# Performance work log

Hardware: AMD Instinct MI355X
Metric: run time of the kernel (lower is better)

## Reference

```python
import jax, jax.numpy as jnp
import numpy as np

N, B, D = 2048, 2, 512
H, R = 8, 3
C = D // H  # head dim = 64


def setup_inputs() -> dict:
    key = jax.random.key(0)
    ks = jax.random.split(key, 12)
    x_q = jax.random.normal(ks[0], (N, B, D), jnp.float32)
    x_k = jax.random.normal(ks[1], (N, B, D), jnp.float32)
    x_v = jax.random.normal(ks[2], (N, B, D), jnp.float32)
    attn_mask = jax.random.randint(ks[3], (B, R, N, N), 0, 2).astype(bool)
    # pad the last 128 key positions (realistic padding; avoids all -inf rows)
    key_padding_mask = jnp.zeros((B, N), bool).at[:, -128:].set(True)
    s = 1.0 / np.sqrt(D)
    Wq = jax.random.normal(ks[4], (D, D), jnp.float32) * s
    Wk = jax.random.normal(ks[5], (D, D), jnp.float32) * s
    Wv = jax.random.normal(ks[6], (D, D), jnp.float32) * s
    Wo = jax.random.normal(ks[7], (D, D), jnp.float32) * s
    bq = jnp.zeros((D,), jnp.float32)
    bk = jnp.zeros((D,), jnp.float32)
    bv = jnp.zeros((D,), jnp.float32)
    bo = jnp.zeros((D,), jnp.float32)
    # mask_weight: randn, last column set to sqrt(head_dim) as in __init__
    mask_weight = jax.random.normal(ks[8], (H, R + 1), jnp.float32)
    mask_weight = mask_weight.at[:, -1].set(np.sqrt(C))
    return dict(x_q=x_q, x_k=x_k, x_v=x_v, attn_mask=attn_mask,
                key_padding_mask=key_padding_mask, Wq=Wq, bq=bq, Wk=Wk, bk=bk,
                Wv=Wv, bv=bv, Wo=Wo, bo=bo, mask_weight=mask_weight)


def _split_heads(x):
    # (n, b, h*c) -> (b, h, n, c)
    n, b, _ = x.shape
    return jnp.transpose(x.reshape(n, b, H, C), (1, 2, 0, 3))


def reference(x_q, x_k, x_v, attn_mask, key_padding_mask,
              Wq, bq, Wk, bk, Wv, bv, Wo, bo, mask_weight):
    q = _split_heads(x_q @ Wq + bq)  # (b,h,n,c)
    k = _split_heads(x_k @ Wk + bk)
    v = _split_heads(x_v @ Wv + bv)

    # relative bias: softmax over edge-type weights, scaled per head
    rel_w = jax.nn.softmax(mask_weight[:, :-1], axis=-1)  # (h,r)
    inv_mask = (~attn_mask).astype(jnp.float32)           # (b,r,n,m)
    rel = jnp.einsum('hr,h,brnm->bhnm', rel_w, mask_weight[:, -1], inv_mask)
    rel = jnp.where(key_padding_mask[:, None, None, :], -jnp.inf, rel)

    # scaled dot-product attention (torch default scale = 1/sqrt(head_dim))
    scores = jnp.einsum('bhnc,bhmc->bhnm', q, k) * (1.0 / np.sqrt(C))
    attn = jax.nn.softmax(scores + rel, axis=-1)
    o = jnp.einsum('bhnm,bhmc->bhnc', attn, v)

    # (b,h,n,c) -> (n,b,h*c)
    n = o.shape[2]
    o = jnp.transpose(o, (2, 0, 1, 3)).reshape(n, o.shape[0], H * C)
    return o @ Wo + bo
```

## Files before the change

kernel.cpp:

```cpp
#include <hip/hip_runtime.h>
#include <hip/hip_bf16.h>

#define NN 2048
#define LOG2E 1.4426950408889634f

typedef unsigned int u32;
typedef unsigned short u16;
typedef unsigned char u8;

typedef __attribute__((ext_vector_type(8))) short short8;
typedef __attribute__((ext_vector_type(4))) float f32x4;

__device__ __forceinline__ u16 f2bf(float f){
  __hip_bfloat16 h = __float2bfloat16(f);
  return *reinterpret_cast<u16*>(&h);
}
__device__ __forceinline__ u32 pack2(float a, float b){
  return (u32)f2bf(a) | ((u32)f2bf(b) << 16);
}

__global__ __launch_bounds__(256)
void prep_k(const int* __restrict__ am, const int* __restrict__ kp,
            u8* __restrict__ cmb)
{
  const size_t tid  = (size_t)blockIdx.x * 256 + threadIdx.x;
  const size_t base = tid * 4;
  const int row = (int)(base >> 11);
  const int m0  = (int)(base & 2047);
  const int b = row >> 11, n = row & 2047;
  const size_t e0 = (((size_t)(b*3) * NN) + n) * NN + m0;
  const int4 a0 = *reinterpret_cast<const int4*>(am + e0);
  const int4 a1 = *reinterpret_cast<const int4*>(am + e0 + (size_t)NN*NN);
  const int4 a2 = *reinterpret_cast<const int4*>(am + e0 + 2*(size_t)NN*NN);
  const int4 kv = *reinterpret_cast<const int4*>(kp + (size_t)b*NN + m0);
  const int a0v[4] = {a0.x,a0.y,a0.z,a0.w};
  const int a1v[4] = {a1.x,a1.y,a1.z,a1.w};
  const int a2v[4] = {a2.x,a2.y,a2.z,a2.w};
  const int kvv[4] = {kv.x,kv.y,kv.z,kv.w};
  uchar4 out;
  u8* o = (u8*)&out;
  #pragma unroll
  for (int i = 0; i < 4; ++i)
    o[i] = (u8)((a0v[i]?1:0) | (a1v[i]?2:0) | (a2v[i]?4:0) | (kvv[i]?8:0));
  *reinterpret_cast<uchar4*>(cmb + base) = out;
}

__global__ __launch_bounds__(256)
void trw_k(const float* __restrict__ W, u16* __restrict__ WT)
{
  __shared__ float tile[32][33];
  const int t = threadIdx.x;
  const int k0 = blockIdx.x * 32, n0 = blockIdx.y * 32;
  const int c = t & 31, r = t >> 5;
  #pragma unroll
  for (int i = 0; i < 4; ++i)
    tile[r + 8*i][c] = W[(size_t)(k0 + r + 8*i) * 512 + n0 + c];
  __syncthreads();
  #pragma unroll
  for (int i = 0; i < 4; ++i)
    WT[(size_t)(n0 + r + 8*i) * 512 + k0 + c] = f2bf(tile[c][r + 8*i]);
}

template<int BN, bool SCATTER, bool ABF16, bool OUTF32>
__device__ __forceinline__
void gemm_core(const void* __restrict__ Av, const u16* __restrict__ WT,
               const float* __restrict__ bias, void* __restrict__ Cd,
               float scale, int m0, int n0)
{
  constexpr int NI  = BN / 64;
  constexpr int WNL = BN / 32;
  __shared__ u16 As[2][64*64];
  __shared__ u16 Ws[2][BN*64];

  const int t = threadIdx.x;
  const int lane = t & 63;
  const int w = t >> 6;
  const int g = lane >> 4, r15 = lane & 15;
  const int wn = w * (BN/4);

  const int arow = t >> 2, akc = (t & 3) * 16, as0 = (t & 3) * 2;
  const int wrn = (BN==128) ? (t>>1) : (t>>2);
  const int wkc = (BN==128) ? ((t&1)*32) : ((t&3)*16);
  const int wsb = (BN==128) ? ((t&1)*4)  : ((t&3)*2);

  uint4  war[WNL];
  uint4  aab[2];
  float4 aaf[4];

  auto loadA = [&](int k0){
    if constexpr (ABF16) {
      const u16* A = (const u16*)Av;
      aab[0] = *reinterpret_cast<const uint4*>(A + (size_t)(m0+arow)*512 + k0 + akc);
      aab[1] = *reinterpret_cast<const uint4*>(A + (size_t)(m0+arow)*512 + k0 + akc + 8);
    } else {
      const float* A = (const float*)Av;
      #pragma unroll
      for (int q = 0; q < 4; ++q)
        aaf[q] = *reinterpret_cast<const float4*>(A + (size_t)(m0+arow)*512 + k0 + akc + 4*q);
    }
  };
  auto loadW = [&](int k0){
    #pragma unroll
    for (int i = 0; i < WNL; ++i)
      war[i] = *reinterpret_cast<const uint4*>(WT + (size_t)(n0+wrn)*512 + k0 + wkc + 8*i);
  };
  auto writeA = [&](int bf){
    uint4 v0, v1;
    if constexpr (ABF16) { v0 = aab[0]; v1 = aab[1]; }
    else {
      v0.x = pack2(aaf[0].x, aaf[0].y); v0.y = pack2(aaf[0].z, aaf[0].w);
      v0.z = pack2(aaf[1].x, aaf[1].y); v0.w = pack2(aaf[1].z, aaf[1].w);
      v1.x = pack2(aaf[2].x, aaf[2].y); v1.y = pack2(aaf[2].z, aaf[2].w);
      v1.z = pack2(aaf[3].x, aaf[3].y); v1.w = pack2(aaf[3].z, aaf[3].w);
    }
    *reinterpret_cast<uint4*>(&As[bf][arow*64 + (((as0  ) ^ (arow&7)) << 3)]) = v0;
    *reinterpret_cast<uint4*>(&As[bf][arow*64 + (((as0+1) ^ (arow&7)) << 3)]) = v1;
  };
  auto writeW = [&](int bf){
    #pragma unroll
    for (int i = 0; i < WNL; ++i)
      *reinterpret_cast<uint4*>(&Ws[bf][wrn*64 + (((wsb+i) ^ (wrn&7)) << 3)]) = war[i];
  };

  const f32x4 fz = {0.f,0.f,0.f,0.f};
  f32x4 acc[4][NI];
  #pragma unroll
  for (int mi = 0; mi < 4; ++mi)
    #pragma unroll
    for (int ni = 0; ni < NI; ++ni) acc[mi][ni] = fz;

  loadA(0); loadW(0);
  writeA(0); writeW(0);
  __syncthreads();

  for (int kt = 0; kt < 8; ++kt) {
    const int cur = kt & 1;
    if (kt < 7) { loadA((kt+1)*64); loadW((kt+1)*64); }
    #pragma unroll
    for (int ks = 0; ks < 2; ++ks) {
      short8 bfr[NI], afr[4];
      #pragma unroll
      for (int ni = 0; ni < NI; ++ni) {
        const int n = wn + 16*ni + r15;
        bfr[ni] = *reinterpret_cast<const short8*>(&Ws[cur][n*64 + (((ks*4+g) ^ (n&7)) << 3)]);
      }
      #pragma unroll
      for (int mi = 0; mi < 4; ++mi) {
        const int m = 16*mi + r15;
        afr[mi] = *reinterpret_cast<const short8*>(&As[cur][m*64 + (((ks*4+g) ^ (m&7)) << 3)]);
      }
      #pragma unroll
      for (int mi = 0; mi < 4; ++mi)
        #pragma unroll
        for (int ni = 0; ni < NI; ++ni)
          acc[mi][ni] = __builtin_amdgcn_mfma_f32_16x16x32_bf16(afr[mi], bfr[ni], acc[mi][ni], 0, 0, 0);
    }
    if (kt < 7) { writeA(cur^1); writeW(cur^1); }
    __syncthreads();
  }

  float bia[NI];
  #pragma unroll
  for (int ni = 0; ni < NI; ++ni) bia[ni] = bias[n0 + wn + 16*ni + r15];
  #pragma unroll
  for (int mi = 0; mi < 4; ++mi) {
    #pragma unroll
    for (int ni = 0; ni < NI; ++ni) {
      #pragma unroll
      for (int j = 0; j < 4; ++j) {
        const int row = m0 + 16*mi + 4*g + j;
        const int col = n0 + wn + 16*ni + r15;
        const float v = (acc[mi][ni][j] + bia[ni]) * scale;
        if constexpr (SCATTER) {
          const int bb = row & 1, ntok = row >> 1;
          const int h = col >> 6, c = col & 63;
          ((u16*)Cd)[(((size_t)(bb*8 + h) * NN + ntok) * 64) + c] = f2bf(v);
        } else if constexpr (OUTF32) {
          ((float*)Cd)[(size_t)row * 512 + col] = v;
        } else {
          ((u16*)Cd)[(size_t)row * 512 + col] = f2bf(v);
        }
      }
    }
  }
}

__global__ __launch_bounds__(256)
void gemm_qkv(const float* __restrict__ x0, const float* __restrict__ x1,
              const float* __restrict__ x2, const u16* __restrict__ WT3,
              const float* __restrict__ b0, const float* __restrict__ b1,
              const float* __restrict__ b2, u16* __restrict__ dst, float qscale)
{
  const int z = blockIdx.z;
  const float* A    = (z == 0) ? x0 : (z == 1) ? x1 : x2;
  const float* bias = (z == 0) ? b0 : (z == 1) ? b1 : b2;
  gemm_core<128, true, false, false>(A, WT3 + (size_t)z*262144, bias,
                                     dst + (size_t)z*2097152,
                                     (z == 0) ? qscale : 1.0f,
                                     blockIdx.x*64, blockIdx.y*128);
}

__global__ __launch_bounds__(256)
void gemm_wo(const u16* __restrict__ Ob, const u16* __restrict__ WT,
             const float* __restrict__ bias, float* __restrict__ out)
{
  gemm_core<64, false, true, true>(Ob, WT, bias, out, 1.0f,
                                   blockIdx.x*64, blockIdx.y*64);
}

__global__ __launch_bounds__(512)
void attn_mfma(const u16* __restrict__ Q, const u16* __restrict__ K,
               const u16* __restrict__ V, const u8* __restrict__ cmb,
               const float* __restrict__ mw, u16* __restrict__ O,
               float* __restrict__ Opart, float2* __restrict__ Ml, int kspan)
{
  __shared__ u16 Ks[2][64*64];
  __shared__ u16 Vs[2][64*64];
  __shared__ u16 Ps[8][16*64];
  __shared__ float lut[16];

  const int t = threadIdx.x;
  const int lane = t & 63;
  const int w = t >> 6;
  const int g = lane >> 4;
  const int r15 = lane & 15;
  const int bh = blockIdx.y;
  const int z = blockIdx.z;
  const int b = bh >> 3, h = bh & 7;
  const int n0 = blockIdx.x * 128;
  const int nq = n0 + w*16 + r15;
  const int k_beg = z * kspan;
  const float NEGINF = -__builtin_inff();

  if (t < 16) {
    const float mw0 = mw[h*4+0], mw1 = mw[h*4+1], mw2 = mw[h*4+2];
    const float msc = mw[h*4+3];
    const float mxw = fmaxf(mw0, fmaxf(mw1, mw2));
    const float e0 = __expf(mw0-mxw), e1 = __expf(mw1-mxw), e2 = __expf(mw2-mxw);
    const float inv = msc / (e0+e1+e2);
    float v = ((t & 1) ? 0.f : e0*inv) + ((t & 2) ? 0.f : e1*inv)
            + ((t & 4) ? 0.f : e2*inv);
    lut[t] = (t & 8) ? NEGINF : v * LOG2E;
  }

  const u16* qrow = Q + ((size_t)bh*NN + nq)*64;
  const short8 bq0 = *reinterpret_cast<const short8*>(qrow + 8*g);
  const short8 bq1 = *reinterpret_cast<const short8*>(qrow + 32 + 8*g);

  const u8* crow = cmb + ((size_t)(b*NN + nq))*NN;
  const u16* Kbase = K + (size_t)bh*NN*64;
  const u16* Vbase = V + (size_t)bh*NN*64;

  float m_run = NEGINF, l_run = 0.f;
  const f32x4 fz = {0.f, 0.f, 0.f, 0.f};
  f32x4 oacc[4] = {fz, fz, fz, fz};

  const int sm  = t >> 3;
  const int sc0 = (t & 7) * 8;
  const int ss  = t & 7;

  uint4 kreg, vreg;
  auto loadKV = [&](int m0){
    kreg = *reinterpret_cast<const uint4*>(Kbase + (size_t)(m0 + sm)*64 + sc0);
    vreg = *reinterpret_cast<const uint4*>(Vbase + (size_t)(m0 + sm)*64 + sc0);
  };
  auto writeKV = [&](int bf){
    *reinterpret_cast<uint4*>(&Ks[bf][sm*64 + ((ss ^ (sm & 7)) << 3)]) = kreg;
    u16 e[8];
    e[0]=vreg.x&0xffff; e[1]=vreg.x>>16; e[2]=vreg.y&0xffff; e[3]=vreg.y>>16;
    e[4]=vreg.z&0xffff; e[5]=vreg.z>>16; e[6]=vreg.w&0xffff; e[7]=vreg.w>>16;
    #pragma unroll
    for (int i = 0; i < 8; ++i) {
      const int c = sc0 + i;
      Vs[bf][c*64 + ((((sm>>3) ^ (c&7) ^ (c>>3)) << 3) | (sm & 7))] = e[i];
    }
  };

  const int ntiles = kspan >> 6;
  loadKV(k_beg);
  writeKV(0);
  __syncthreads();

  for (int it = 0; it < ntiles; ++it) {
    const int cur = it & 1;
    const int m0 = k_beg + it * 64;
    const bool more = (it + 1 < ntiles);
    if (more) loadKV(m0 + 64);

    f32x4 sac[4];
    #pragma unroll
    for (int kt = 0; kt < 4; ++kt) {
      const int key = 16*kt + r15;
      const short8 a0 = *reinterpret_cast<const short8*>(&Ks[cur][key*64 + (((g  ) ^ (key&7)) << 3)]);
      const short8 a1 = *reinterpret_cast<const short8*>(&Ks[cur][key*64 + (((g+4) ^ (key&7)) << 3)]);
      f32x4 s = fz;
      s = __builtin_amdgcn_mfma_f32_16x16x32_bf16(a0, bq0, s, 0, 0, 0);
      s = __builtin_amdgcn_mfma_f32_16x16x32_bf16(a1, bq1, s, 0, 0, 0);
      sac[kt] = s;
    }

    float sv[4][4];
    float pmax = NEGINF;
    #pragma unroll
    for (int kt = 0; kt < 4; ++kt) {
      const u32 cw = *reinterpret_cast<const u32*>(crow + m0 + 16*kt + 4*g);
      #pragma unroll
      for (int j = 0; j < 4; ++j) {
        const u32 ci = (cw >> (8*j)) & 0xffu;
        sv[kt][j] = sac[kt][j] + lut[ci];
        pmax = fmaxf(pmax, sv[kt][j]);
      }
    }
    float tmax = pmax;
    tmax = fmaxf(tmax, __shfl_xor(tmax, 16));
    tmax = fmaxf(tmax, __shfl_xor(tmax, 32));

    const float nm = fmaxf(m_run, tmax);
    float sc;
    if (nm == NEGINF) { sc = 1.f; }
    else { sc = exp2f(m_run - nm); m_run = nm; }

    float psum = 0.f;
    #pragma unroll
    for (int kt = 0; kt < 4; ++kt) {
      float p[4];
      #pragma unroll
      for (int j = 0; j < 4; ++j) {
        p[j] = (nm == NEGINF) ? 0.f : exp2f(sv[kt][j] - nm);
        psum += p[j];
      }
      const int slot = 2*kt + (g >> 1);
      const int off  = 4 * (g & 1);
      *reinterpret_cast<ushort4*>(&Ps[w][r15*64 + ((slot ^ (r15 & 7)) << 3) + off]) =
        make_ushort4(f2bf(p[0]), f2bf(p[1]), f2bf(p[2]), f2bf(p[3]));
    }
    psum += __shfl_xor(psum, 16);
    psum += __shfl_xor(psum, 32);
    l_run = l_run * sc + psum;
    #pragma unroll
    for (int ct = 0; ct < 4; ++ct) oacc[ct] *= sc;

    const short8 bp0 = *reinterpret_cast<const short8*>(&Ps[w][r15*64 + (((g  ) ^ (r15 & 7)) << 3)]);
    const short8 bp1 = *reinterpret_cast<const short8*>(&Ps[w][r15*64 + (((g+4) ^ (r15 & 7)) << 3)]);
    #pragma unroll
    for (int ct = 0; ct < 4; ++ct) {
      const int c = 16*ct + r15;
      const int sw0 = (g  ) ^ (c&7) ^ (c>>3);
      const int sw1 = (g+4) ^ (c&7) ^ (c>>3);
      const short8 av0 = *reinterpret_cast<const short8*>(&Vs[cur][c*64 + (sw0 << 3)]);
      const short8 av1 = *reinterpret_cast<const short8*>(&Vs[cur][c*64 + (sw1 << 3)]);
      oacc[ct] = __builtin_amdgcn_mfma_f32_16x16x32_bf16(av0, bp0, oacc[ct], 0, 0, 0);
      oacc[ct] = __builtin_amdgcn_mfma_f32_16x16x32_bf16(av1, bp1, oacc[ct], 0, 0, 0);
    }

    if (more) writeKV(cur ^ 1);
    __syncthreads();
  }

  if (Opart) {
    float* orow = Opart + (((size_t)(z*16 + bh)) * NN + nq) * 64;
    #pragma unroll
    for (int ct = 0; ct < 4; ++ct)
      *reinterpret_cast<float4*>(orow + 16*ct + 4*g) =
        make_float4(oacc[ct][0], oacc[ct][1], oacc[ct][2], oacc[ct][3]);
    if (g == 0)
      Ml[((size_t)(z*16 + bh)) * NN + nq] = make_float2(m_run, l_run);
  } else {
    const float rinv = 1.f / l_run;
    #pragma unroll
    for (int ct = 0; ct < 4; ++ct) {
      u16* dst = O + ((size_t)(nq*2 + b))*512 + h*64 + 16*ct + 4*g;
      *reinterpret_cast<ushort4*>(dst) =
        make_ushort4(f2bf(oacc[ct][0]*rinv), f2bf(oacc[ct][1]*rinv),
                     f2bf(oacc[ct][2]*rinv), f2bf(oacc[ct][3]*rinv));
    }
  }
}

__global__ __launch_bounds__(256)
void combine_k(const float* __restrict__ Opart, const float2* __restrict__ Ml,
               u16* __restrict__ Ob, int nsplit)
{
  const int t = threadIdx.x;
  const int lane = t & 63, w = t >> 6;
  const int q = blockIdx.x * 4 + w;
  const int bh = blockIdx.y;
  const int b = bh >> 3, h = bh & 7;

  float M = -__builtin_inff();
  for (int s = 0; s < nsplit; ++s)
    M = fmaxf(M, Ml[((size_t)(s*16 + bh)) * NN + q].x);

  float num = 0.f, den = 0.f;
  for (int s = 0; s < nsplit; ++s) {
    const float2 ml = Ml[((size_t)(s*16 + bh)) * NN + q];
    const float ws = (ml.x == -__builtin_inff()) ? 0.f : exp2f(ml.x - M);
    den += ws * ml.y;
    num += ws * Opart[(((size_t)(s*16 + bh)) * NN + q) * 64 + lane];
  }
  const float r = (den > 0.f) ? num / den : 0.f;
  Ob[((size_t)(q*2 + b)) * 512 + h*64 + lane] = f2bf(r);
}

extern "C" void kernel_launch(void* const* d_in, const int* in_sizes, int n_in,
                              void* d_out, int out_size, void* d_ws, size_t ws_size,
                              hipStream_t stream)
{
  const float* xq = (const float*)d_in[0];
  const float* xk = (const float*)d_in[1];
  const float* xv = (const float*)d_in[2];
  const int*   am = (const int*)d_in[3];
  const int*   kp = (const int*)d_in[4];
  const float* Wq = (const float*)d_in[5];
  const float* bq = (const float*)d_in[6];
  const float* Wk = (const float*)d_in[7];
  const float* bk = (const float*)d_in[8];
  const float* Wv = (const float*)d_in[9];
  const float* bv = (const float*)d_in[10];
  const float* Wo = (const float*)d_in[11];
  const float* bo = (const float*)d_in[12];
  const float* mw = (const float*)d_in[13];

  u16* Qb = (u16*)d_ws;
  u16* Kb = Qb + (size_t)16*NN*64;
  u16* Vb = Kb + (size_t)16*NN*64;
  u16* Ob = Vb + (size_t)16*NN*64;
  u8*  cmb = (u8*)(Ob + (size_t)4096*512);
  u8*  R   = cmb + (size_t)2*NN*NN;

  u16*   WT3   = (u16*)R;
  float* Opart = (float*)R;
  const size_t base_bytes = (size_t)(R - (u8*)d_ws);
  int nsplit = 1;
  for (int s = 4; s >= 1; s >>= 1) {
    const size_t need = base_bytes + (size_t)s * 16 * NN * (64*4 + 8);
    if (need <= ws_size) { nsplit = s; break; }
  }
  float2* Ml = (float2*)(Opart + (size_t)nsplit * 16 * NN * 64);
  const bool split = (base_bytes + (size_t)16*NN*(64*4+8) <= ws_size) &&
                     (base_bytes + (size_t)3*512*512*2 <= ws_size);
  u16* WTo = Qb;

  prep_k<<<(2*NN*NN/4 + 255)/256, 256, 0, stream>>>(am, kp, cmb);

  const float qscale = 0.125f * LOG2E;
  if (split) {
    trw_k<<<dim3(16, 16), 256, 0, stream>>>(Wq, WT3);
    trw_k<<<dim3(16, 16), 256, 0, stream>>>(Wk, WT3 + 262144);
    trw_k<<<dim3(16, 16), 256, 0, stream>>>(Wv, WT3 + 2*262144);
    gemm_qkv<<<dim3(64, 4, 3), 256, 0, stream>>>(xq, xk, xv, WT3, bq, bk, bv, Qb, qscale);
    attn_mfma<<<dim3(16, 16, nsplit), 512, 0, stream>>>(Qb, Kb, Vb, cmb, mw, Ob,
                                                        Opart, Ml, NN / nsplit);
    combine_k<<<dim3(NN/4, 16), 256, 0, stream>>>(Opart, Ml, Ob, nsplit);
    trw_k<<<dim3(16, 16), 256, 0, stream>>>(Wo, WTo);
    gemm_wo<<<dim3(64, 8), 256, 0, stream>>>(Ob, WTo, bo, (float*)d_out);
  } else {
    trw_k<<<dim3(16, 16), 256, 0, stream>>>(Wq, WT3);
    gemm_qkv<<<dim3(64, 4, 1), 256, 0, stream>>>(xq, xk, xv, WT3, bq, bk, bv, Qb, qscale);
    trw_k<<<dim3(16, 16), 256, 0, stream>>>(Wk, WT3);
    gemm_qkv<<<dim3(64, 4, 1), 256, 0, stream>>>(xk, xk, xv, WT3 - 262144, bk, bk, bv, Kb - 0, qscale);
    attn_mfma<<<dim3(16, 16, 1), 512, 0, stream>>>(Qb, Kb, Vb, cmb, mw, Ob,
                                                   nullptr, nullptr, NN);
    trw_k<<<dim3(16, 16), 256, 0, stream>>>(Wo, WTo);
    gemm_wo<<<dim3(64, 8), 256, 0, stream>>>(Ob, WTo, bo, (float*)d_out);
  }
}
```

Before: 130.5 us.

## Rework attention inner loop: direct-to-LDS K loads, register P shuffle, lazy rescale

```diff
diff --git a/kernel.cpp b/kernel.cpp
--- a/kernel.cpp
+++ b/kernel.cpp
@@ -17,6 +17,10 @@
 }
 __device__ __forceinline__ u32 pack2(float a, float b){
   return (u32)f2bf(a) | ((u32)f2bf(b) << 16);
+}
+__device__ __forceinline__ void gload16(const void* g, void* l){
+  __builtin_amdgcn_global_load_lds((const __attribute__((address_space(1))) u32*)g,
+                                   (__attribute__((address_space(3))) u32*)l, 16, 0, 0);
 }
 
 __global__ __launch_bounds__(256)
@@ -46,6 +50,25 @@
 }
 
 __global__ __launch_bounds__(256)
+void trw3_k(const float* __restrict__ W0, const float* __restrict__ W1,
+            const float* __restrict__ W2, u16* __restrict__ WT)
+{
+  __shared__ float tile[32][33];
+  const float* W = (blockIdx.z == 0) ? W0 : (blockIdx.z == 1) ? W1 : W2;
+  u16* dst = WT + (size_t)blockIdx.z * 262144;
+  const int t = threadIdx.x;
+  const int k0 = blockIdx.x * 32, n0 = blockIdx.y * 32;
+  const int c = t & 31, r = t >> 5;
+  #pragma unroll
+  for (int i = 0; i < 4; ++i)
+    tile[r + 8*i][c] = W[(size_t)(k0 + r + 8*i) * 512 + n0 + c];
+  __syncthreads();
+  #pragma unroll
+  for (int i = 0; i < 4; ++i)
+    dst[(size_t)(n0 + r + 8*i) * 512 + k0 + c] = f2bf(tile[c][r + 8*i]);
+}
+
+__global__ __launch_bounds__(256)
 void trw_k(const float* __restrict__ W, u16* __restrict__ WT)
 {
   __shared__ float tile[32][33];
@@ -208,7 +231,7 @@
                                    blockIdx.x*64, blockIdx.y*64);
 }
 
-__global__ __launch_bounds__(512)
+__global__ __launch_bounds__(512, 8)
 void attn_mfma(const u16* __restrict__ Q, const u16* __restrict__ K,
                const u16* __restrict__ V, const u8* __restrict__ cmb,
                const float* __restrict__ mw, u16* __restrict__ O,
@@ -216,7 +239,6 @@
 {
   __shared__ u16 Ks[2][64*64];
   __shared__ u16 Vs[2][64*64];
-  __shared__ u16 Ps[8][16*64];
   __shared__ float lut[16];
 
   const int t = threadIdx.x;
@@ -256,16 +278,20 @@
   f32x4 oacc[4] = {fz, fz, fz, fz};
 
   const int sm  = t >> 3;
+  const int ssl = t & 7;
+  const int kcol = (ssl ^ (sm & 7)) * 8;
   const int sc0 = (t & 7) * 8;
-  const int ss  = t & 7;
-
-  uint4 kreg, vreg;
-  auto loadKV = [&](int m0){
-    kreg = *reinterpret_cast<const uint4*>(Kbase + (size_t)(m0 + sm)*64 + sc0);
+  const int aA = (((g & 1) << 5) + r15) << 2;
+  const int aB = aA + 64;
+
+  uint4 vreg;
+  auto gloadK = [&](int m0, int bf){
+    gload16(Kbase + (size_t)(m0 + sm)*64 + kcol, &Ks[bf][w*512 + (lane << 3)]);
+  };
+  auto loadV = [&](int m0){
     vreg = *reinterpret_cast<const uint4*>(Vbase + (size_t)(m0 + sm)*64 + sc0);
   };
-  auto writeKV = [&](int bf){
-    *reinterpret_cast<uint4*>(&Ks[bf][sm*64 + ((ss ^ (sm & 7)) << 3)]) = kreg;
+  auto writeV = [&](int bf){
     u16 e[8];
     e[0]=vreg.x&0xffff; e[1]=vreg.x>>16; e[2]=vreg.y&0xffff; e[3]=vreg.y>>16;
     e[4]=vreg.z&0xffff; e[5]=vreg.z>>16; e[6]=vreg.w&0xffff; e[7]=vreg.w>>16;
@@ -277,17 +303,18 @@
   };
 
   const int ntiles = kspan >> 6;
-  loadKV(k_beg);
-  writeKV(0);
+  gloadK(k_beg, 0);
+  loadV(k_beg);
+  writeV(0);
   __syncthreads();
 
   for (int it = 0; it < ntiles; ++it) {
     const int cur = it & 1;
     const int m0 = k_beg + it * 64;
     const bool more = (it + 1 < ntiles);
-    if (more) loadKV(m0 + 64);
-
-    f32x4 sac[4];
+    if (more) { gloadK(m0 + 64, cur ^ 1); loadV(m0 + 64); }
+
+    float sv[4][4];
     #pragma unroll
     for (int kt = 0; kt < 4; ++kt) {
       const int key = 16*kt + r15;
@@ -296,64 +323,102 @@
       f32x4 s = fz;
       s = __builtin_amdgcn_mfma_f32_16x16x32_bf16(a0, bq0, s, 0, 0, 0);
       s = __builtin_amdgcn_mfma_f32_16x16x32_bf16(a1, bq1, s, 0, 0, 0);
-      sac[kt] = s;
-    }
-
-    float sv[4][4];
+      const u32 cw = *reinterpret_cast<const u32*>(crow + m0 + 16*kt + 4*g);
+      #pragma unroll
+      for (int j = 0; j < 4; ++j)
+        sv[kt][j] = s[j] + lut[(cw >> (8*j)) & 0xfu];
+    }
     float pmax = NEGINF;
     #pragma unroll
-    for (int kt = 0; kt < 4; ++kt) {
-      const u32 cw = *reinterpret_cast<const u32*>(crow + m0 + 16*kt + 4*g);
-      #pragma unroll
-      for (int j = 0; j < 4; ++j) {
-        const u32 ci = (cw >> (8*j)) & 0xffu;
-        sv[kt][j] = sac[kt][j] + lut[ci];
-        pmax = fmaxf(pmax, sv[kt][j]);
-      }
-    }
+    for (int kt = 0; kt < 4; ++kt)
+      #pragma unroll
+      for (int j = 0; j < 4; ++j) pmax = fmaxf(pmax, sv[kt][j]);
     float tmax = pmax;
     tmax = fmaxf(tmax, __shfl_xor(tmax, 16));
     tmax = fmaxf(tmax, __shfl_xor(tmax, 32));
 
-    const float nm = fmaxf(m_run, tmax);
-    float sc;
-    if (nm == NEGINF) { sc = 1.f; }
-    else { sc = exp2f(m_run - nm); m_run = nm; }
+    const bool skip = __all((m_run != NEGINF) && (tmax <= m_run + 10.0f));
+    float nm = m_run, sc = 1.0f;
+    if (!skip) {
+      nm = fmaxf(m_run, tmax);
+      if (nm != NEGINF) { sc = exp2f(m_run - nm); m_run = nm; }
+      #pragma unroll
+      for (int ct = 0; ct < 4; ++ct) oacc[ct] *= sc;
+    }
 
     float psum = 0.f;
-    #pragma unroll
-    for (int kt = 0; kt < 4; ++kt) {
-      float p[4];
-      #pragma unroll
-      for (int j = 0; j < 4; ++j) {
-        p[j] = (nm == NEGINF) ? 0.f : exp2f(sv[kt][j] - nm);
-        psum += p[j];
-      }
-      const int slot = 2*kt + (g >> 1);
-      const int off  = 4 * (g & 1);
-      *reinterpret_cast<ushort4*>(&Ps[w][r15*64 + ((slot ^ (r15 & 7)) << 3) + off]) =
-        make_ushort4(f2bf(p[0]), f2bf(p[1]), f2bf(p[2]), f2bf(p[3]));
-    }
+    const bool hig = (g >= 2);
+
+    {
+      u32 wp[2][2];
+      #pragma unroll
+      for (int kt = 0; kt < 2; ++kt) {
+        float p[4];
+        #pragma unroll
+        for (int j = 0; j < 4; ++j) {
+          p[j] = (nm == NEGINF) ? 0.f : exp2f(sv[kt][j] - nm);
+          psum += p[j];
+        }
+        wp[kt][0] = pack2(p[0], p[1]);
+        wp[kt][1] = pack2(p[2], p[3]);
+      }
+      const u32 e0 = __builtin_amdgcn_ds_bpermute(aA, (int)wp[0][0]);
+      const u32 e1 = __builtin_amdgcn_ds_bpermute(aA, (int)wp[0][1]);
+      const u32 e2 = __builtin_amdgcn_ds_bpermute(aB, (int)wp[0][0]);
+      const u32 e3 = __builtin_amdgcn_ds_bpermute(aB, (int)wp[0][1]);
+      const u32 f0 = __builtin_amdgcn_ds_bpermute(aA, (int)wp[1][0]);
+      const u32 f1 = __builtin_amdgcn_ds_bpermute(aA, (int)wp[1][1]);
+      const u32 f2 = __builtin_amdgcn_ds_bpermute(aB, (int)wp[1][0]);
+      const u32 f3 = __builtin_amdgcn_ds_bpermute(aB, (int)wp[1][1]);
+      union { uint4 u; short8 s; } cv;
+      cv.u = make_uint4(hig ? f0 : e0, hig ? f1 : e1, hig ? f2 : e2, hig ? f3 : e3);
+      const short8 bp0 = cv.s;
+      #pragma unroll
+      for (int ct = 0; ct < 4; ++ct) {
+        const int c = 16*ct + r15;
+        const short8 av0 = *reinterpret_cast<const short8*>(
+          &Vs[cur][c*64 + ((((g  ) ^ (c&7) ^ (c>>3))) << 3)]);
+        oacc[ct] = __builtin_amdgcn_mfma_f32_16x16x32_bf16(av0, bp0, oacc[ct], 0, 0, 0);
+      }
+    }
+    {
+      u32 wp[2][2];
+      #pragma unroll
+      for (int kt = 0; kt < 2; ++kt) {
+        float p[4];
+        #pragma unroll
+        for (int j = 0; j < 4; ++j) {
+          p[j] = (nm == NEGINF) ? 0.f : exp2f(sv[kt+2][j] - nm);
+          psum += p[j];
+        }
+        wp[kt][0] = pack2(p[0], p[1]);
+        wp[kt][1] = pack2(p[2], p[3]);
+      }
+      const u32 e0 = __builtin_amdgcn_ds_bpermute(aA, (int)wp[0][0]);
+      const u32 e1 = __builtin_amdgcn_ds_bpermute(aA, (int)wp[0][1]);
+      const u32 e2 = __builtin_amdgcn_ds_bpermute(aB, (int)wp[0][0]);
+      const u32 e3 = __builtin_amdgcn_ds_bpermute(aB, (int)wp[0][1]);
+      const u32 f0 = __builtin_amdgcn_ds_bpermute(aA, (int)wp[1][0]);
+      const u32 f1 = __builtin_amdgcn_ds_bpermute(aA, (int)wp[1][1]);
+      const u32 f2 = __builtin_amdgcn_ds_bpermute(aB, (int)wp[1][0]);
+      const u32 f3 = __builtin_amdgcn_ds_bpermute(aB, (int)wp[1][1]);
+      union { uint4 u; short8 s; } cv;
+      cv.u = make_uint4(hig ? f0 : e0, hig ? f1 : e1, hig ? f2 : e2, hig ? f3 : e3);
+      const short8 bp1 = cv.s;
+      #pragma unroll
+      for (int ct = 0; ct < 4; ++ct) {
+        const int c = 16*ct + r15;
+        const short8 av1 = *reinterpret_cast<const short8*>(
+          &Vs[cur][c*64 + ((((g+4) ^ (c&7) ^ (c>>3))) << 3)]);
+        oacc[ct] = __builtin_amdgcn_mfma_f32_16x16x32_bf16(av1, bp1, oacc[ct], 0, 0, 0);
+      }
+    }
+
     psum += __shfl_xor(psum, 16);
     psum += __shfl_xor(psum, 32);
     l_run = l_run * sc + psum;
-    #pragma unroll
-    for (int ct = 0; ct < 4; ++ct) oacc[ct] *= sc;
-
-    const short8 bp0 = *reinterpret_cast<const short8*>(&Ps[w][r15*64 + (((g  ) ^ (r15 & 7)) << 3)]);
-    const short8 bp1 = *reinterpret_cast<const short8*>(&Ps[w][r15*64 + (((g+4) ^ (r15 & 7)) << 3)]);
-    #pragma unroll
-    for (int ct = 0; ct < 4; ++ct) {
-      const int c = 16*ct + r15;
-      const int sw0 = (g  ) ^ (c&7) ^ (c>>3);
-      const int sw1 = (g+4) ^ (c&7) ^ (c>>3);
-      const short8 av0 = *reinterpret_cast<const short8*>(&Vs[cur][c*64 + (sw0 << 3)]);
-      const short8 av1 = *reinterpret_cast<const short8*>(&Vs[cur][c*64 + (sw1 << 3)]);
-      oacc[ct] = __builtin_amdgcn_mfma_f32_16x16x32_bf16(av0, bp0, oacc[ct], 0, 0, 0);
-      oacc[ct] = __builtin_amdgcn_mfma_f32_16x16x32_bf16(av1, bp1, oacc[ct], 0, 0, 0);
-    }
-
-    if (more) writeKV(cur ^ 1);
+
+    if (more) writeV(cur ^ 1);
     __syncthreads();
   }
 
@@ -444,24 +509,17 @@
   prep_k<<<(2*NN*NN/4 + 255)/256, 256, 0, stream>>>(am, kp, cmb);
 
   const float qscale = 0.125f * LOG2E;
+  trw3_k<<<dim3(16, 16, 3), 256, 0, stream>>>(Wq, Wk, Wv, WT3);
+  gemm_qkv<<<dim3(64, 4, 3), 256, 0, stream>>>(xq, xk, xv, WT3, bq, bk, bv, Qb, qscale);
+
   if (split) {
-    trw_k<<<dim3(16, 16), 256, 0, stream>>>(Wq, WT3);
-    trw_k<<<dim3(16, 16), 256, 0, stream>>>(Wk, WT3 + 262144);
-    trw_k<<<dim3(16, 16), 256, 0, stream>>>(Wv, WT3 + 2*262144);
-    gemm_qkv<<<dim3(64, 4, 3), 256, 0, stream>>>(xq, xk, xv, WT3, bq, bk, bv, Qb, qscale);
     attn_mfma<<<dim3(16, 16, nsplit), 512, 0, stream>>>(Qb, Kb, Vb, cmb, mw, Ob,
                                                         Opart, Ml, NN / nsplit);
     combine_k<<<dim3(NN/4, 16), 256, 0, stream>>>(Opart, Ml, Ob, nsplit);
-    trw_k<<<dim3(16, 16), 256, 0, stream>>>(Wo, WTo);
-    gemm_wo<<<dim3(64, 8), 256, 0, stream>>>(Ob, WTo, bo, (float*)d_out);
   } else {
-    trw_k<<<dim3(16, 16), 256, 0, stream>>>(Wq, WT3);
-    gemm_qkv<<<dim3(64, 4, 1), 256, 0, stream>>>(xq, xk, xv, WT3, bq, bk, bv, Qb, qscale);
-    trw_k<<<dim3(16, 16), 256, 0, stream>>>(Wk, WT3);
-    gemm_qkv<<<dim3(64, 4, 1), 256, 0, stream>>>(xk, xk, xv, WT3 - 262144, bk, bk, bv, Kb - 0, qscale);
     attn_mfma<<<dim3(16, 16, 1), 512, 0, stream>>>(Qb, Kb, Vb, cmb, mw, Ob,
                                                    nullptr, nullptr, NN);
-    trw_k<<<dim3(16, 16), 256, 0, stream>>>(Wo, WTo);
-    gemm_wo<<<dim3(64, 8), 256, 0, stream>>>(Ob, WTo, bo, (float*)d_out);
-  }
-}
+  }
+  trw_k<<<dim3(16, 16), 256, 0, stream>>>(Wo, WTo);
+  gemm_wo<<<dim3(64, 8), 256, 0, stream>>>(Ob, WTo, bo, (float*)d_out);
+}
```

Result: slower. 222.1 us (+70.1%).
